# Kernel optimization log

Measured on AMD Instinct MI355X. Metric: run time of the kernel, lower is better.

The kernel has to match this reference:

```python
import jax, jax.numpy as jnp
import numpy as np
from jax import lax

FH, FW = 38, 63          # feature map H,W (600x1000 image, stride 16)
A = 9                    # anchors per location (3 scales x 3 ratios)
POOL = 7                 # cfg.POOLING_SIZE
PRE_NMS, POST_NMS = 6000, 300
NMS_THRESH = 0.7
IM_H, IM_W = 600.0, 1000.0
STRIDE = 16.0


def _make_anchors(h, w, stride=16):
    ratios = np.array([0.5, 1.0, 2.0]); scales = np.array([8.0, 16.0, 32.0])
    base = 16.0; ctr = (base - 1.0) / 2.0
    ws = np.round(np.sqrt(base * base / ratios)); hs = np.round(ws * ratios)
    ws = (ws[:, None] * scales[None, :]).ravel(); hs = (hs[:, None] * scales[None, :]).ravel()
    ba = np.stack([ctr - 0.5 * (ws - 1), ctr - 0.5 * (hs - 1),
                   ctr + 0.5 * (ws - 1), ctr + 0.5 * (hs - 1)], 1)
    sx, sy = np.meshgrid(np.arange(w) * stride, np.arange(h) * stride)
    shifts = np.stack([sx.ravel(), sy.ravel(), sx.ravel(), sy.ravel()], 1)
    return (shifts[:, None, :] + ba[None]).reshape(-1, 4).astype(np.float32)


def _conv(x, w, b, pad):
    y = lax.conv_general_dilated(x, w, (1, 1), pad,
                                 dimension_numbers=('NCHW', 'OIHW', 'NCHW'))
    return y + b[None, :, None, None]


def _bbox_transform_inv(anchors, deltas):
    w = anchors[:, 2] - anchors[:, 0] + 1.0
    h = anchors[:, 3] - anchors[:, 1] + 1.0
    cx = anchors[:, 0] + 0.5 * w
    cy = anchors[:, 1] + 0.5 * h
    dx, dy, dw, dh = deltas[:, 0], deltas[:, 1], deltas[:, 2], deltas[:, 3]
    pcx = dx * w + cx; pcy = dy * h + cy
    pw = jnp.exp(dw) * w; ph = jnp.exp(dh) * h
    return jnp.stack([pcx - 0.5 * pw, pcy - 0.5 * ph,
                      pcx + 0.5 * pw, pcy + 0.5 * ph], 1)


def _nms_keep(boxes, thresh):
    # greedy NMS over score-sorted boxes, fixed-size keep mask
    x1, y1, x2, y2 = boxes[:, 0], boxes[:, 1], boxes[:, 2], boxes[:, 3]
    areas = (x2 - x1 + 1.0) * (y2 - y1 + 1.0)
    iw = jnp.maximum(jnp.minimum(x2[:, None], x2[None, :])
                     - jnp.maximum(x1[:, None], x1[None, :]) + 1.0, 0.0)
    ih = jnp.maximum(jnp.minimum(y2[:, None], y2[None, :])
                     - jnp.maximum(y1[:, None], y1[None, :]) + 1.0, 0.0)
    inter = iw * ih
    iou = inter / (areas[:, None] + areas[None, :] - inter)
    n = boxes.shape[0]; ar = jnp.arange(n)
    def body(i, keep):
        sup = (iou[i] > thresh) & (ar > i) & keep[i]
        return keep & ~sup
    return lax.fori_loop(0, n, body, jnp.ones((n,), bool))


def _crop_and_resize(feat, boxes, crop):
    # feat [C,H,W]; boxes [R,4] normalized (y1,x1,y2,x2); TF crop_and_resize semantics
    C, H, W = feat.shape
    t = jnp.arange(crop, dtype=feat.dtype) / (crop - 1)
    def one(box):
        by1, bx1, by2, bx2 = box
        ys = by1 * (H - 1) + t * (by2 - by1) * (H - 1)
        xs = bx1 * (W - 1) + t * (bx2 - bx1) * (W - 1)
        y0f = jnp.floor(ys); x0f = jnp.floor(xs)
        wy = (ys - y0f)[None, :, None]; wx = (xs - x0f)[None, None, :]
        y0 = jnp.clip(y0f, 0, H - 1).astype(jnp.int32)
        y1i = jnp.clip(y0f + 1, 0, H - 1).astype(jnp.int32)
        x0 = jnp.clip(x0f, 0, W - 1).astype(jnp.int32)
        x1i = jnp.clip(x0f + 1, 0, W - 1).astype(jnp.int32)
        f00 = feat[:, y0][:, :, x0]; f01 = feat[:, y0][:, :, x1i]
        f10 = feat[:, y1i][:, :, x0]; f11 = feat[:, y1i][:, :, x1i]
        return (f00 * (1 - wy) * (1 - wx) + f01 * (1 - wy) * wx
                + f10 * wy * (1 - wx) + f11 * wy * wx)
    return jax.vmap(one)(boxes)


def _forward(net_conv, w_rpn, b_rpn, w_cls, b_cls, w_bbox, b_bbox, anchors):
    # _region_proposal: 3x3 rpn conv + relu, 1x1 cls / bbox heads
    rpn = jax.nn.relu(_conv(net_conv, w_rpn, b_rpn, 'SAME'))
    cls = _conv(rpn, w_cls, b_cls, 'VALID')    # [1,2A,H,W]
    bbox = _conv(rpn, w_bbox, b_bbox, 'VALID')  # [1,4A,H,W]
    # view(1,2,-1,W) softmax: channel a pairs with channel a+A (bg/fg)
    bg, fg = cls[:, :A], cls[:, A:]
    fg_prob = jax.nn.softmax(jnp.stack([bg, fg], axis=1), axis=1)[:, 1]  # [1,A,H,W]
    scores = jnp.transpose(fg_prob, (0, 2, 3, 1)).reshape(-1)            # (H*W*A,)
    deltas = jnp.transpose(bbox, (0, 2, 3, 1)).reshape(-1, 4)
    proposals = _bbox_transform_inv(anchors, deltas)
    proposals = jnp.stack([jnp.clip(proposals[:, 0], 0.0, IM_W - 1.0),
                           jnp.clip(proposals[:, 1], 0.0, IM_H - 1.0),
                           jnp.clip(proposals[:, 2], 0.0, IM_W - 1.0),
                           jnp.clip(proposals[:, 3], 0.0, IM_H - 1.0)], 1)
    # proposal selection is non-differentiable (rois.detach() in original)
    scores_sg = lax.stop_gradient(scores)
    props_sg = lax.stop_gradient(proposals)
    _, order = lax.top_k(scores_sg, PRE_NMS)
    boxes = props_sg[order]
    keep = _nms_keep(boxes, NMS_THRESH)
    idx = jnp.sort(jnp.where(keep, jnp.arange(PRE_NMS), PRE_NMS))[:POST_NMS]
    rois = boxes[jnp.minimum(idx, PRE_NMS - 1)]  # [300,4] (x1,y1,x2,y2)
    # _crop_pool_layer with max_pool=True: crop to 14x14 then 2x2 max pool
    H, W = net_conv.shape[2], net_conv.shape[3]
    x1 = rois[:, 0] / STRIDE; y1 = rois[:, 1] / STRIDE
    x2 = rois[:, 2] / STRIDE; y2 = rois[:, 3] / STRIDE
    norm = jnp.stack([y1 / (H - 1), x1 / (W - 1), y2 / (H - 1), x2 / (W - 1)], 1)
    crops = _crop_and_resize(net_conv[0], norm, 2 * POOL)  # [300,C,14,14]
    R, C = crops.shape[0], crops.shape[1]
    return crops.reshape(R, C, POOL, 2, POOL, 2).max(axis=(3, 5))  # [300,C,7,7]


def setup_inputs():
    key = jax.random.key(0)
    ks = jax.random.split(key, 4)
    net_conv = jax.random.normal(ks[0], (1, 512, FH, FW), jnp.float32)
    w_rpn = jax.random.normal(ks[1], (512, 512, 3, 3), jnp.float32) * 0.01
    b_rpn = jnp.zeros((512,), jnp.float32)
    w_cls = jax.random.normal(ks[2], (2 * A, 512, 1, 1), jnp.float32) * 0.01
    b_cls = jnp.zeros((2 * A,), jnp.float32)
    w_bbox = jax.random.normal(ks[3], (4 * A, 512, 1, 1), jnp.float32) * 0.01
    b_bbox = jnp.zeros((4 * A,), jnp.float32)
    anchors = jnp.asarray(_make_anchors(FH, FW))
    return {"net_conv": net_conv, "w_rpn": w_rpn, "b_rpn": b_rpn,
            "w_cls": w_cls, "b_cls": b_cls, "w_bbox": w_bbox,
            "b_bbox": b_bbox, "anchors": anchors}


def reference(net_conv, w_rpn, b_rpn, w_cls, b_cls, w_bbox, b_bbox, anchors):
    return _forward(net_conv, w_rpn, b_rpn, w_cls, b_cls, w_bbox, b_bbox, anchors)
```

## Files before the change

### kernel.cpp

```cpp
#include <hip/hip_runtime.h>
#include <stdint.h>

#define NPOS 2394
#define CIN 512
#define KK 4608
#define NANCH 21546
#define PRE 6000
#define POST 300
#define NWORD 94
#define NQ 8
#define QLEN 2694
#define FEATT_BYTES 4902912

#define OFF_BH    0
#define OFF_BL    4718592
#define OFF_P0    9437184
#define OFF_SBOX  9437184
#define OFF_KEEP  9533440
#define OFF_DIAG  9633792
#define OFF_P1    14340096
#define OFF_KEYS  19243008
#define OFF_PROP  19415552
#define OFF_RPART 19760384
#define OFF_FPH   20450048
#define OFF_FPL   23179264

typedef _Float16 half8 __attribute__((ext_vector_type(8)));
typedef float f32x4 __attribute__((ext_vector_type(4)));

__device__ __forceinline__ void gload16(const void* g, void* l) {
    __builtin_amdgcn_global_load_lds((const __attribute__((address_space(1))) void*)g,
                                     (__attribute__((address_space(3))) void*)l, 16, 0, 0);
}

__device__ __forceinline__ unsigned long long rl64(unsigned long long v, int l) {
    union { unsigned long long q; unsigned int d[2]; } s; s.q = v;
    unsigned int lo = __builtin_amdgcn_readlane(s.d[0], l);
    unsigned int hi = __builtin_amdgcn_readlane(s.d[1], l);
    return ((unsigned long long)hi << 32) | (unsigned long long)lo;
}

__global__ __launch_bounds__(256) void k_transpose_feat(const float* __restrict__ in,
                                                        float* __restrict__ featT) {
    __shared__ float tl[32][33];
    int tx = threadIdx.x & 31, tg = threadIdx.x >> 5;
    int posBase = blockIdx.x * 32, ciBase = blockIdx.y * 32;
#pragma unroll
    for (int j = 0; j < 4; ++j) {
        int ci = ciBase + tg + j * 8;
        int pos = posBase + tx;
        tl[tg + j * 8][tx] = (pos < NPOS) ? in[(size_t)ci * NPOS + pos] : 0.f;
    }
    __syncthreads();
#pragma unroll
    for (int j = 0; j < 4; ++j) {
        int pos = posBase + tg + j * 8;
        int ci = ciBase + tx;
        if (pos < NPOS) featT[(size_t)pos * 512 + ci] = tl[tx][tg + j * 8];
    }
}

__global__ void k_pad_split(const float* __restrict__ featT,
                            _Float16* __restrict__ FPH, _Float16* __restrict__ FPL) {
    int idx = blockIdx.x * 256 + threadIdx.x;
    int ci = idx & 511;
    int rc = idx >> 9;
    int hp = rc / 65, wp = rc - hp * 65;
    int h = hp - 1, w = wp - 1;
    float a = 0.f;
    if ((unsigned)h < 38u && (unsigned)w < 63u)
        a = featT[(size_t)(h * 63 + w) * 512 + ci] * 16.f;
    _Float16 ah = (_Float16)a;
    _Float16 al = (_Float16)(a - (float)ah);
    FPH[idx] = ah; FPL[idx] = al;
}

__global__ void k_prep_wf16(const float* __restrict__ w,
                            _Float16* __restrict__ BH, _Float16* __restrict__ BL) {
    int idx = blockIdx.x * 256 + threadIdx.x;
    int co = idx / KK;
    int rem = idx - co * KK;
    int p = rem >> 9;
    int ci = rem & 511;
    float b = w[(co * CIN + ci) * 9 + p] * 128.f;
    _Float16 bh = (_Float16)b;
    _Float16 bl = (_Float16)(b - (float)bh);
    BH[idx] = bh; BL[idx] = bl;
}

__global__ __launch_bounds__(256, 3) void k_conv3_mfma(
    const _Float16* __restrict__ FPH, const _Float16* __restrict__ FPL,
    const _Float16* __restrict__ BHp, const _Float16* __restrict__ BLp,
    float* __restrict__ P0, float* __restrict__ P1)
{
    __shared__ __align__(16) char lds[49152];
    const int t = threadIdx.x;
    const int wave = t >> 6, lane = t & 63;
    const int posBase = blockIdx.x * 128;
    const int coBase  = blockIdx.y * 64;
    const int z = blockIdx.z;
    float* __restrict__ P = z ? P1 : P0;
    const int wm = wave >> 1, wn = wave & 1;
    const int lr = lane & 15, lg = lane >> 4;

    int addrA[4][2], addrB[2][2];
#pragma unroll
    for (int m = 0; m < 4; ++m) {
        int row = wm * 64 + m * 16 + lr;
        int x = row & 7;
        addrA[m][0] = row * 128 + ((lg ^ x) << 4);
        addrA[m][1] = row * 128 + (((4 + lg) ^ x) << 4);
    }
#pragma unroll
    for (int n = 0; n < 2; ++n) {
        int row = wn * 32 + n * 16 + lr;
        int x = row & 7;
        addrB[n][0] = 32768 + row * 128 + ((lg ^ x) << 4);
        addrB[n][1] = 32768 + row * 128 + (((4 + lg) ^ x) << 4);
    }

    int baseA[4], ldsAo[4];
#pragma unroll
    for (int s = 0; s < 4; ++s) {
        int row = (wave * 4 + s) * 8 + (lane >> 3);
        int pos = posBase + row;
        int h = pos / 63;
        int w = pos - h * 63;
        int swz = ((lane & 7) ^ (row & 7)) * 8;
        baseA[s] = (h * 65 + w) * 512 + swz;
        ldsAo[s] = (wave * 4 + s) * 1024 + lane * 16;
    }
    int baseB[2], ldsBo[2];
#pragma unroll
    for (int s = 0; s < 2; ++s) {
        int row = (wave * 2 + s) * 8 + (lane >> 3);
        int swz = ((lane & 7) ^ (row & 7)) * 8;
        baseB[s] = (coBase + row) * KK + swz;
        ldsBo[s] = 32768 + (wave * 2 + s) * 1024 + lane * 16;
    }

    f32x4 acc[4][2];
#pragma unroll
    for (int m = 0; m < 4; ++m)
#pragma unroll
        for (int n = 0; n < 2; ++n) acc[m][n] = (f32x4){0.f, 0.f, 0.f, 0.f};

    const int kbeg = z * 2304;
    for (int step = 0; step < 36; ++step) {
        int k0 = kbeg + step * 64;
        int p = k0 >> 9;
        int ci0 = k0 & 511;
        int kh = p / 3;
        int kw = p - kh * 3;
        int dA = (kh * 65 + kw) * 512 + ci0;
#pragma unroll
        for (int s = 0; s < 4; ++s) {
            int so = baseA[s] + dA;
            gload16(FPH + so, lds + ldsAo[s]);
            gload16(FPL + so, lds + 16384 + ldsAo[s]);
        }
#pragma unroll
        for (int s = 0; s < 2; ++s) {
            int so = baseB[s] + k0;
            gload16(BHp + so, lds + ldsBo[s]);
            gload16(BLp + so, lds + 8192 + ldsBo[s]);
        }
        __syncthreads();
#pragma unroll
        for (int ks = 0; ks < 2; ++ks) {
            half8 aH[4], aL[4], bH[2], bL[2];
#pragma unroll
            for (int m = 0; m < 4; ++m) {
                aH[m] = *(const half8*)(lds + addrA[m][ks]);
                aL[m] = *(const half8*)(lds + 16384 + addrA[m][ks]);
            }
#pragma unroll
            for (int n = 0; n < 2; ++n) {
                bH[n] = *(const half8*)(lds + addrB[n][ks]);
                bL[n] = *(const half8*)(lds + 8192 + addrB[n][ks]);
            }
#pragma unroll
            for (int m = 0; m < 4; ++m)
#pragma unroll
                for (int n = 0; n < 2; ++n) {
                    acc[m][n] = __builtin_amdgcn_mfma_f32_16x16x32_f16(aH[m], bH[n], acc[m][n], 0, 0, 0);
                    acc[m][n] = __builtin_amdgcn_mfma_f32_16x16x32_f16(aH[m], bL[n], acc[m][n], 0, 0, 0);
                    acc[m][n] = __builtin_amdgcn_mfma_f32_16x16x32_f16(aL[m], bH[n], acc[m][n], 0, 0, 0);
                }
        }
        __syncthreads();
    }

#pragma unroll
    for (int m = 0; m < 4; ++m) {
        int pbase = posBase + wm * 64 + m * 16 + lg * 4;
        int co = coBase + wn * 32 + lr;
#pragma unroll
        for (int r = 0; r < 4; ++r) {
            int pos = pbase + r;
            if (pos < NPOS) {
                P[(size_t)pos * 512 + co]      = acc[m][0][r] * (1.f / 2048.f);
                P[(size_t)pos * 512 + co + 16] = acc[m][1][r] * (1.f / 2048.f);
            }
        }
    }
}

__global__ __launch_bounds__(256) void k_heads(const float* __restrict__ P0,
                                               const float* __restrict__ P1,
                                               const float* __restrict__ brpn,
                                               const float* __restrict__ wcls,
                                               const float* __restrict__ bcls,
                                               const float* __restrict__ wbbox,
                                               const float* __restrict__ bbbox,
                                               const float* __restrict__ anchors,
                                               float* __restrict__ proposals,
                                               unsigned long long* __restrict__ keys) {
    __shared__ float x[512];
    __shared__ float part[54][4];
    __shared__ float logit[54];
    int pos = blockIdx.x;
    int t = threadIdx.x;
    {
        float v0 = P0[(size_t)pos * 512 + t] + P1[(size_t)pos * 512 + t] + brpn[t];
        float v1 = P0[(size_t)pos * 512 + t + 256] + P1[(size_t)pos * 512 + t + 256] + brpn[t + 256];
        x[t] = v0 > 0.f ? v0 : 0.f;
        x[t + 256] = v1 > 0.f ? v1 : 0.f;
    }
    __syncthreads();
    if (t < 216) {
        int o = t >> 2, q = t & 3;
        const float* wr = (o < 18) ? (wcls + o * 512) : (wbbox + (o - 18) * 512);
        float s = 0.f;
        int base = q * 128;
#pragma unroll 4
        for (int k2 = 0; k2 < 128; ++k2) s += x[base + k2] * wr[base + k2];
        part[o][q] = s;
    }
    __syncthreads();
    if (t < 54) {
        float b = (t < 18) ? bcls[t] : bbbox[t - 18];
        logit[t] = part[t][0] + part[t][1] + part[t][2] + part[t][3] + b;
    }
    __syncthreads();
    if (t < 9) {
        int a = t;
        float bg = logit[a], fg = logit[9 + a];
        float score = 1.f / (1.f + expf(bg - fg));
        float dx = logit[18 + 4 * a], dy = logit[19 + 4 * a];
        float dw = logit[20 + 4 * a], dh = logit[21 + 4 * a];
        int idx = pos * 9 + a;
        float ax1 = anchors[idx * 4 + 0], ay1 = anchors[idx * 4 + 1];
        float ax2 = anchors[idx * 4 + 2], ay2 = anchors[idx * 4 + 3];
        float aw = ax2 - ax1 + 1.f, ah = ay2 - ay1 + 1.f;
        float cx = ax1 + 0.5f * aw, cy = ay1 + 0.5f * ah;
        float pcx = dx * aw + cx, pcy = dy * ah + cy;
        float pw = expf(dw) * aw, ph = expf(dh) * ah;
        float x1 = fminf(fmaxf(pcx - 0.5f * pw, 0.f), 999.f);
        float y1 = fminf(fmaxf(pcy - 0.5f * ph, 0.f), 599.f);
        float x2 = fminf(fmaxf(pcx + 0.5f * pw, 0.f), 999.f);
        float y2 = fminf(fmaxf(pcy + 0.5f * ph, 0.f), 599.f);
        proposals[idx * 4 + 0] = x1; proposals[idx * 4 + 1] = y1;
        proposals[idx * 4 + 2] = x2; proposals[idx * 4 + 3] = y2;
        union { float f; unsigned int i; } sv; sv.f = score;
        keys[idx] = (((unsigned long long)sv.i) << 32) |
                    (unsigned long long)(0xFFFFFFFFu - (unsigned)idx);
    }
}

__global__ __launch_bounds__(256) void k_rank_partial(const unsigned long long* __restrict__ keys,
                                                      unsigned int* __restrict__ rpart) {
    __shared__ unsigned long long kc[1024];
    int i = blockIdx.x * 256 + threadIdx.x;
    int q = blockIdx.y;
    unsigned long long myk = (i < NANCH) ? keys[i] : 0xFFFFFFFFFFFFFFFFull;
    int j0 = q * QLEN;
    int j1 = j0 + QLEN; if (j1 > NANCH) j1 = NANCH;
    unsigned int cnt = 0;
    for (int base = j0; base < j1; base += 1024) {
        int nload = j1 - base; if (nload > 1024) nload = 1024;
        __syncthreads();
        for (int u = threadIdx.x; u < 1024; u += 256)
            kc[u] = (base + u < j1) ? keys[base + u] : 0ull;
        __syncthreads();
        for (int u = 0; u < nload; ++u)
            cnt += (kc[u] > myk) ? 1u : 0u;
    }
    if (i < NANCH) rpart[i * NQ + q] = cnt;
}

__global__ void k_zero_aux(float* __restrict__ sboxes, unsigned long long* __restrict__ diag4) {
    int i = blockIdx.x * 256 + threadIdx.x;
    diag4[i] = 0ull;
    if (i < PRE * 4) sboxes[i] = 0.f;
}

__global__ void k_rank_scatter(const unsigned int* __restrict__ rpart,
                               const float* __restrict__ proposals,
                               float* __restrict__ sboxes) {
    int i = blockIdx.x * 256 + threadIdx.x;
    if (i >= NANCH) return;
    unsigned int r = 0;
#pragma unroll
    for (int q = 0; q < NQ; q++) r += rpart[i * NQ + q];
    if (r < PRE) {
        sboxes[r * 4 + 0] = proposals[i * 4 + 0];
        sboxes[r * 4 + 1] = proposals[i * 4 + 1];
        sboxes[r * 4 + 2] = proposals[i * 4 + 2];
        sboxes[r * 4 + 3] = proposals[i * 4 + 3];
    }
}

__global__ __launch_bounds__(64) void k_nms_mask(const float* __restrict__ sboxes,
                                                 unsigned long long* __restrict__ mask,
                                                 unsigned long long* __restrict__ diag4) {
    __shared__ float bx[64][4];
    int ib = blockIdx.x, jb = blockIdx.y;
    int lane = threadIdx.x;
    int j = jb * 64 + lane;
    if (j < PRE) {
        bx[lane][0] = sboxes[j * 4 + 0]; bx[lane][1] = sboxes[j * 4 + 1];
        bx[lane][2] = sboxes[j * 4 + 2]; bx[lane][3] = sboxes[j * 4 + 3];
    } else {
        bx[lane][0] = 3e8f; bx[lane][1] = 3e8f; bx[lane][2] = 3e8f; bx[lane][3] = 3e8f;
    }
    __syncthreads();
    int i = ib * 64 + lane;
    if (i >= PRE) return;
    float x1 = sboxes[i * 4 + 0], y1 = sboxes[i * 4 + 1];
    float x2 = sboxes[i * 4 + 2], y2 = sboxes[i * 4 + 3];
    float ar = (x2 - x1 + 1.f) * (y2 - y1 + 1.f);
    unsigned long long bits = 0;
#pragma unroll 4
    for (int u = 0; u < 64; u++) {
        int j2 = jb * 64 + u;
        float iw = fminf(x2, bx[u][2]) - fmaxf(x1, bx[u][0]) + 1.f;
        float ih = fminf(y2, bx[u][3]) - fmaxf(y1, bx[u][1]) + 1.f;
        iw = fmaxf(iw, 0.f); ih = fmaxf(ih, 0.f);
        float inter = iw * ih;
        float arj = (bx[u][2] - bx[u][0] + 1.f) * (bx[u][3] - bx[u][1] + 1.f);
        float iou = inter / (ar + arj - inter);
        if (iou > 0.7f && j2 > i) bits |= (1ull << u);
    }
    mask[(size_t)i * NWORD + jb] = bits;
    if ((jb >> 2) == (ib >> 2)) diag4[(size_t)i * 4 + (jb & 3)] = bits;
}

#define NSB 24
#define SBW 256
#define NSLOT 20
__global__ __launch_bounds__(64) void k_nms_scan(const unsigned long long* __restrict__ mask,
                                                 const unsigned long long* __restrict__ diag4,
                                                 int* __restrict__ keep) {
    __shared__ __align__(16) unsigned long long tile[2][SBW * 4];
    __shared__ __align__(16) char ldsrow[NSLOT * 1024];
    __shared__ int ldsk[POST];
    const int lane = threadIdx.x;
    const char* dg = (const char*)diag4;

    for (int c = 0; c < 8; ++c)
        gload16(dg + c * 1024 + (size_t)lane * 16, (char*)tile[0] + c * 1024);

    unsigned long long rem0 = 0, rem1 = 0;
    int nk = 0, npend = 0;

    for (int sb = 0; sb < NSB; ++sb) {
        if (sb + 1 < NSB) {
            const char* src = dg + (size_t)(sb + 1) * 8192;
            char* dst = (char*)tile[(sb + 1) & 1];
            for (int c = 0; c < 8; ++c)
                gload16(src + c * 1024 + (size_t)lane * 16, dst + c * 1024);
            asm volatile("s_waitcnt vmcnt(8)" ::: "memory");
        } else {
            asm volatile("s_waitcnt vmcnt(0)" ::: "memory");
        }
        __builtin_amdgcn_sched_barrier(0);

        for (int q = 0; q < npend; ++q) {
            const unsigned long long* lr = (const unsigned long long*)(ldsrow + q * 1024);
            rem0 |= lr[lane];
            if (lane < NWORD - 64) rem1 |= lr[64 + lane];
        }
        npend = 0;

        const unsigned long long* tl = tile[sb & 1];
        unsigned long long d[4][4];
#pragma unroll
        for (int q = 0; q < 4; ++q) {
            ulonglong2 e0 = *(const ulonglong2*)&tl[(q * 64 + lane) * 4];
            ulonglong2 e1 = *(const ulonglong2*)&tl[(q * 64 + lane) * 4 + 2];
            d[q][0] = e0.x; d[q][1] = e0.y; d[q][2] = e1.x; d[q][3] = e1.y;
        }

        const int w0 = 4 * sb;
        const int base = sb * SBW;
        unsigned long long rmw[4];
#pragma unroll
        for (int j = 0; j < 4; ++j) {
            int w = w0 + j;
            rmw[j] = (w < 64) ? rl64(rem0, w) : ((w < NWORD) ? rl64(rem1, w - 64) : ~0ull);
        }

#pragma unroll
        for (int p = 0; p < 4; ++p) {
            int w = w0 + p;
            if (w >= NWORD) break;
            const unsigned long long valid = (w == NWORD - 1) ? ((1ull << 48) - 1) : ~0ull;
            unsigned long long above = ~0ull;
            unsigned long long keptm = 0;
            for (;;) {
                unsigned long long a = ~rmw[p] & valid & above;
                if (!a) break;
                int u = (int)(__ffsll((long long)a) - 1);
                keptm |= 1ull << u;
                ++nk;
#pragma unroll
                for (int j = p; j < 4; ++j) rmw[j] |= rl64(d[p][j], u);
                if (nk == POST) break;
                above = (u == 63) ? 0ull : (~0ull << (u + 1));
            }
            unsigned long long bits = keptm;
            int nkb = nk - __builtin_popcountll(keptm);
            while (bits) {
                int u = (int)(__ffsll((long long)bits) - 1); bits &= bits - 1;
                int i = base + p * 64 + u;
                if (lane == 0) ldsk[nkb] = i;
                ++nkb;
                if (npend == NSLOT) {
                    asm volatile("s_waitcnt vmcnt(0)" ::: "memory");
                    __builtin_amdgcn_sched_barrier(0);
                    for (int q = 0; q < NSLOT; ++q) {
                        const unsigned long long* lr = (const unsigned long long*)(ldsrow + q * 1024);
                        rem0 |= lr[lane];
                        if (lane < NWORD - 64) rem1 |= lr[64 + lane];
                    }
                    npend = 0;
                }
                gload16((const char*)(mask + (size_t)i * NWORD) + (size_t)lane * 16,
                        ldsrow + npend * 1024);
                ++npend;
            }
            if (nk >= POST) goto done;
        }
    }
done:
    asm volatile("s_waitcnt vmcnt(0)" ::: "memory");
    for (int k2 = lane; k2 < POST; k2 += 64)
        keep[k2] = (k2 < nk) ? ldsk[k2] : PRE - 1;
}

__global__ __launch_bounds__(256) void k_gather_rois(const float* sboxes, const int* keep,
                                                     float* outF) {
    int t = threadIdx.x;
    float4 box[2];
    int nr = 0;
    for (int r = t; r < POST; r += 256) {
        int ki = keep[r];
        if (ki < 0) ki = 0; if (ki > PRE - 1) ki = PRE - 1;
        box[nr++] = *reinterpret_cast<const float4*>(sboxes + ki * 4);
    }
    __syncthreads();
    nr = 0;
    for (int r = t; r < POST; r += 256) {
        float4 b = box[nr++];
#pragma unroll
        for (int cg = 0; cg < 8; ++cg)
            *reinterpret_cast<float4*>(outF + (size_t)(r * 512 + cg * 64) * 49) = b;
    }
}

__global__ __launch_bounds__(256) void k_crop_fast(const float* __restrict__ featT,
                                                   float* out) {
    __shared__ float lds[4][49 * 65];
    int r = blockIdx.x;
    int w = threadIdx.x >> 6, lane = threadIdx.x & 63;
    int cg = blockIdx.y * 4 + w;
    int c = cg * 64 + lane;
    float* chunk = out + (size_t)(r * 512 + cg * 64) * 49;
    const float4 b = *reinterpret_cast<const float4*>(chunk);
    float x1 = b.x, y1 = b.y, x2 = b.z, y2 = b.w;
    float by1 = (y1 / 16.f) / 37.f, bx1 = (x1 / 16.f) / 62.f;
    float by2 = (y2 / 16.f) / 37.f, bx2 = (x2 / 16.f) / 62.f;
    float dyn = by2 - by1, dxn = bx2 - bx1;
    for (int e = 0; e < 49; ++e) {
        int oy = e / 7, ox = e - oy * 7;
        float vv[4];
#pragma unroll
        for (int dy = 0; dy < 2; ++dy) {
            int sy = 2 * oy + dy;
            float ty = (float)sy / 13.f;
            float ys = by1 * 37.f + (ty * dyn) * 37.f;
            float yf = floorf(ys);
            float wy = ys - yf;
            int y0  = (int)fminf(fmaxf(yf, 0.f), 37.f);
            int y1i = (int)fminf(fmaxf(yf + 1.f, 0.f), 37.f);
#pragma unroll
            for (int dxx = 0; dxx < 2; ++dxx) {
                int sx = 2 * ox + dxx;
                float tx = (float)sx / 13.f;
                float xs = bx1 * 62.f + (tx * dxn) * 62.f;
                float xf = floorf(xs);
                float wx = xs - xf;
                int x0  = (int)fminf(fmaxf(xf, 0.f), 62.f);
                int x1i = (int)fminf(fmaxf(xf + 1.f, 0.f), 62.f);
                float f00 = featT[(size_t)(y0 * 63 + x0) * 512 + c];
                float f01 = featT[(size_t)(y0 * 63 + x1i) * 512 + c];
                float f10 = featT[(size_t)(y1i * 63 + x0) * 512 + c];
                float f11 = featT[(size_t)(y1i * 63 + x1i) * 512 + c];
                vv[dy * 2 + dxx] = f00 * (1.f - wy) * (1.f - wx) + f01 * (1.f - wy) * wx +
                                   f10 * wy * (1.f - wx) + f11 * wy * wx;
            }
        }
        lds[w][e * 65 + lane] = fmaxf(fmaxf(vv[0], vv[1]), fmaxf(vv[2], vv[3]));
    }
    __syncthreads();
    for (int i = lane; i < 64 * 49; i += 64) {
        int cl = i / 49, e = i - cl * 49;
        chunk[i] = lds[w][e * 65 + cl];
    }
}

__global__ __launch_bounds__(64) void k_crop_slow(const float* __restrict__ net,
                                                  float* out) {
    int r = blockIdx.x, cg = blockIdx.y;
    int lane = threadIdx.x;
    int c = cg * 64 + lane;
    const float4 b = *reinterpret_cast<const float4*>(out + (size_t)(r * 512 + cg * 64) * 49);
    float x1 = b.x, y1 = b.y, x2 = b.z, y2 = b.w;
    float by1 = (y1 / 16.f) / 37.f, bx1 = (x1 / 16.f) / 62.f;
    float by2 = (y2 / 16.f) / 37.f, bx2 = (x2 / 16.f) / 62.f;
    float dyn = by2 - by1, dxn = bx2 - bx1;
    const float* fc = net + (size_t)c * NPOS;
    float* orow = out + ((size_t)r * 512 + c) * 49;
    for (int e = 0; e < 49; ++e) {
        int oy = e / 7, ox = e - oy * 7;
        float vv[4];
#pragma unroll
        for (int dy = 0; dy < 2; ++dy) {
            int sy = 2 * oy + dy;
            float ty = (float)sy / 13.f;
            float ys = by1 * 37.f + (ty * dyn) * 37.f;
            float yf = floorf(ys);
            float wy = ys - yf;
            int y0  = (int)fminf(fmaxf(yf, 0.f), 37.f);
            int y1i = (int)fminf(fmaxf(yf + 1.f, 0.f), 37.f);
#pragma unroll
            for (int dxx = 0; dxx < 2; ++dxx) {
                int sx = 2 * ox + dxx;
                float tx = (float)sx / 13.f;
                float xs = bx1 * 62.f + (tx * dxn) * 62.f;
                float xf = floorf(xs);
                float wx = xs - xf;
                int x0  = (int)fminf(fmaxf(xf, 0.f), 62.f);
                int x1i = (int)fminf(fmaxf(xf + 1.f, 0.f), 62.f);
                float f00 = fc[y0 * 63 + x0];
                float f01 = fc[y0 * 63 + x1i];
                float f10 = fc[y1i * 63 + x0];
                float f11 = fc[y1i * 63 + x1i];
                vv[dy * 2 + dxx] = f00 * (1.f - wy) * (1.f - wx) + f01 * (1.f - wy) * wx +
                                   f10 * wy * (1.f - wx) + f11 * wy * wx;
            }
        }
        orow[e] = fmaxf(fmaxf(vv[0], vv[1]), fmaxf(vv[2], vv[3]));
    }
}

extern "C" void kernel_launch(void* const* d_in, const int* in_sizes, int n_in,
                              void* d_out, int out_size, void* d_ws, size_t ws_size,
                              hipStream_t stream) {
    auto find = [&](int count, int fallback) {
        for (int i = 0; i < n_in; ++i) if (in_sizes[i] == count) return i;
        return fallback;
    };
    const float* net   = (const float*)d_in[find(NPOS * CIN, 0)];
    const float* wrpn  = (const float*)d_in[find(512 * KK, 1)];
    const float* brpn  = (const float*)d_in[find(512, 2)];
    const float* wcls  = (const float*)d_in[find(18 * 512, 3)];
    const float* bcls  = (const float*)d_in[find(18, 4)];
    const float* wbbox = (const float*)d_in[find(36 * 512, 5)];
    const float* bbbox = (const float*)d_in[find(36, 6)];
    const float* anch  = (const float*)d_in[find(NANCH * 4, 7)];

    char* ob = (char*)d_out;
    _Float16* BH             = (_Float16*)(ob + OFF_BH);
    _Float16* BL             = (_Float16*)(ob + OFF_BL);
    unsigned long long* mask = (unsigned long long*)(ob + OFF_BH);
    float* P0                = (float*)(ob + OFF_P0);
    float* P1                = (float*)(ob + OFF_P1);
    float* sboxes            = (float*)(ob + OFF_SBOX);
    int* keep                = (int*)(ob + OFF_KEEP);
    unsigned long long* diag4= (unsigned long long*)(ob + OFF_DIAG);
    unsigned long long* keys = (unsigned long long*)(ob + OFF_KEYS);
    float* proposals         = (float*)(ob + OFF_PROP);
    unsigned int* rpart      = (unsigned int*)(ob + OFF_RPART);
    _Float16* FPH            = (_Float16*)(ob + OFF_FPH);
    _Float16* FPL            = (_Float16*)(ob + OFF_FPL);
    float* outF              = (float*)d_out;

    const bool ws_ok = (ws_size >= (size_t)FEATT_BYTES);
    float* featT = ws_ok ? (float*)d_ws : (float*)(ob + OFF_P0);

    hipLaunchKernelGGL(k_transpose_feat, dim3(75, 16), dim3(256), 0, stream, net, featT);
    hipLaunchKernelGGL(k_pad_split, dim3(5330), dim3(256), 0, stream, featT, FPH, FPL);
    hipLaunchKernelGGL(k_prep_wf16, dim3(9216), dim3(256), 0, stream, wrpn, BH, BL);
    hipLaunchKernelGGL(k_conv3_mfma, dim3(19, 8, 2), dim3(256), 0, stream, FPH, FPL, BH, BL, P0, P1);
    hipLaunchKernelGGL(k_heads, dim3(NPOS), dim3(256), 0, stream, P0, P1, brpn, wcls, bcls, wbbox, bbbox, anch, proposals, keys);
    hipLaunchKernelGGL(k_rank_partial, dim3(85, NQ), dim3(256), 0, stream, keys, rpart);
    hipLaunchKernelGGL(k_zero_aux, dim3(96), dim3(256), 0, stream, sboxes, diag4);
    hipLaunchKernelGGL(k_rank_scatter, dim3(85), dim3(256), 0, stream, rpart, proposals, sboxes);
    hipLaunchKernelGGL(k_nms_mask, dim3(NWORD, NWORD), dim3(64), 0, stream, sboxes, mask, diag4);
    hipLaunchKernelGGL(k_nms_scan, dim3(1), dim3(64), 0, stream, mask, diag4, keep);
    hipLaunchKernelGGL(k_gather_rois, dim3(1), dim3(256), 0, stream, sboxes, keep, outF);
    if (ws_ok)
        hipLaunchKernelGGL(k_crop_fast, dim3(POST, 2), dim3(256), 0, stream, featT, outF);
    else
        hipLaunchKernelGGL(k_crop_slow, dim3(POST, 8), dim3(64), 0, stream, net, outF);
}
```

Measured before the change: 410.5 us.

## Split conv K dimension three ways with XCD-aware block swizzle

The 3x3 conv GEMM goes from a 2-way to a 3-way split-K, giving 456 blocks instead of 304 and better filling the device's compute units. A 1-D grid with an (bid&7)*57 remap spreads neighbouring tiles across the XCDs. The heads kernel now sums three partial buffers, which adds global memory traffic. The workspace offsets are rearranged so the extra partial buffer fits, with NMS scratch moved to regions that are no longer in use by then.

```diff
diff --git a/kernel.cpp b/kernel.cpp
--- a/kernel.cpp
+++ b/kernel.cpp
@@ -14,16 +14,18 @@
 
 #define OFF_BH    0
 #define OFF_BL    4718592
-#define OFF_P0    9437184
-#define OFF_SBOX  9437184
-#define OFF_KEEP  9533440
-#define OFF_DIAG  9633792
-#define OFF_P1    14340096
-#define OFF_KEYS  19243008
-#define OFF_PROP  19415552
-#define OFF_RPART 19760384
-#define OFF_FPH   20450048
-#define OFF_FPL   23179264
+#define OFF_FPH   9437184
+#define OFF_FPL   12166144
+#define OFF_P0    14895104
+#define OFF_P1    19798016
+#define OFF_P2    24700928
+#define OFF_KEYS  0
+#define OFF_PROP  180224
+#define OFF_RPART 532480
+#define OFF_SBOX  1228800
+#define OFF_KEEP  1327104
+#define OFF_DIAG  1335296
+#define OFF_MASK  4718592
 
 typedef _Float16 half8 __attribute__((ext_vector_type(8)));
 typedef float f32x4 __attribute__((ext_vector_type(4)));
@@ -91,15 +93,22 @@
 __global__ __launch_bounds__(256, 3) void k_conv3_mfma(
     const _Float16* __restrict__ FPH, const _Float16* __restrict__ FPL,
     const _Float16* __restrict__ BHp, const _Float16* __restrict__ BLp,
-    float* __restrict__ P0, float* __restrict__ P1)
+    float* __restrict__ P0, float* __restrict__ P1, float* __restrict__ P2)
 {
     __shared__ __align__(16) char lds[49152];
     const int t = threadIdx.x;
     const int wave = t >> 6, lane = t & 63;
-    const int posBase = blockIdx.x * 128;
-    const int coBase  = blockIdx.y * 64;
-    const int z = blockIdx.z;
-    float* __restrict__ P = z ? P1 : P0;
+
+    const int bid = blockIdx.x;
+    const int swz = (bid & 7) * 57 + (bid >> 3);
+    const int z = swz / 152;
+    const int rem = swz - z * 152;
+    const int coB = rem / 19;
+    const int posB = rem - coB * 19;
+    const int posBase = posB * 128;
+    const int coBase  = coB * 64;
+    float* __restrict__ P = (z == 0) ? P0 : ((z == 1) ? P1 : P2);
+
     const int wm = wave >> 1, wn = wave & 1;
     const int lr = lane & 15, lg = lane >> 4;
 
@@ -126,16 +135,16 @@
         int pos = posBase + row;
         int h = pos / 63;
         int w = pos - h * 63;
-        int swz = ((lane & 7) ^ (row & 7)) * 8;
-        baseA[s] = (h * 65 + w) * 512 + swz;
+        int swzb = ((lane & 7) ^ (row & 7)) * 8;
+        baseA[s] = (h * 65 + w) * 512 + swzb;
         ldsAo[s] = (wave * 4 + s) * 1024 + lane * 16;
     }
     int baseB[2], ldsBo[2];
 #pragma unroll
     for (int s = 0; s < 2; ++s) {
         int row = (wave * 2 + s) * 8 + (lane >> 3);
-        int swz = ((lane & 7) ^ (row & 7)) * 8;
-        baseB[s] = (coBase + row) * KK + swz;
+        int swzb = ((lane & 7) ^ (row & 7)) * 8;
+        baseB[s] = (coBase + row) * KK + swzb;
         ldsBo[s] = 32768 + (wave * 2 + s) * 1024 + lane * 16;
     }
 
@@ -145,8 +154,8 @@
 #pragma unroll
         for (int n = 0; n < 2; ++n) acc[m][n] = (f32x4){0.f, 0.f, 0.f, 0.f};
 
-    const int kbeg = z * 2304;
-    for (int step = 0; step < 36; ++step) {
+    const int kbeg = z * 1536;
+    for (int step = 0; step < 24; ++step) {
         int k0 = kbeg + step * 64;
         int p = k0 >> 9;
         int ci0 = k0 & 511;
@@ -208,6 +217,7 @@
 
 __global__ __launch_bounds__(256) void k_heads(const float* __restrict__ P0,
                                                const float* __restrict__ P1,
+                                               const float* __restrict__ P2,
                                                const float* __restrict__ brpn,
                                                const float* __restrict__ wcls,
                                                const float* __restrict__ bcls,
@@ -222,8 +232,9 @@
     int pos = blockIdx.x;
     int t = threadIdx.x;
     {
-        float v0 = P0[(size_t)pos * 512 + t] + P1[(size_t)pos * 512 + t] + brpn[t];
-        float v1 = P0[(size_t)pos * 512 + t + 256] + P1[(size_t)pos * 512 + t + 256] + brpn[t + 256];
+        size_t o = (size_t)pos * 512 + t;
+        float v0 = P0[o] + P1[o] + P2[o] + brpn[t];
+        float v1 = P0[o + 256] + P1[o + 256] + P2[o + 256] + brpn[t + 256];
         x[t] = v0 > 0.f ? v0 : 0.f;
         x[t + 256] = v1 > 0.f ? v1 : 0.f;
     }
@@ -584,17 +595,18 @@
     char* ob = (char*)d_out;
     _Float16* BH             = (_Float16*)(ob + OFF_BH);
     _Float16* BL             = (_Float16*)(ob + OFF_BL);
-    unsigned long long* mask = (unsigned long long*)(ob + OFF_BH);
+    _Float16* FPH            = (_Float16*)(ob + OFF_FPH);
+    _Float16* FPL            = (_Float16*)(ob + OFF_FPL);
     float* P0                = (float*)(ob + OFF_P0);
     float* P1                = (float*)(ob + OFF_P1);
+    float* P2                = (float*)(ob + OFF_P2);
+    unsigned long long* keys = (unsigned long long*)(ob + OFF_KEYS);
+    float* proposals         = (float*)(ob + OFF_PROP);
+    unsigned int* rpart      = (unsigned int*)(ob + OFF_RPART);
     float* sboxes            = (float*)(ob + OFF_SBOX);
     int* keep                = (int*)(ob + OFF_KEEP);
     unsigned long long* diag4= (unsigned long long*)(ob + OFF_DIAG);
-    unsigned long long* keys = (unsigned long long*)(ob + OFF_KEYS);
-    float* proposals         = (float*)(ob + OFF_PROP);
-    unsigned int* rpart      = (unsigned int*)(ob + OFF_RPART);
-    _Float16* FPH            = (_Float16*)(ob + OFF_FPH);
-    _Float16* FPL            = (_Float16*)(ob + OFF_FPL);
+    unsigned long long* mask = (unsigned long long*)(ob + OFF_MASK);
     float* outF              = (float*)d_out;
 
     const bool ws_ok = (ws_size >= (size_t)FEATT_BYTES);
@@ -603,8 +615,8 @@
     hipLaunchKernelGGL(k_transpose_feat, dim3(75, 16), dim3(256), 0, stream, net, featT);
     hipLaunchKernelGGL(k_pad_split, dim3(5330), dim3(256), 0, stream, featT, FPH, FPL);
     hipLaunchKernelGGL(k_prep_wf16, dim3(9216), dim3(256), 0, stream, wrpn, BH, BL);
-    hipLaunchKernelGGL(k_conv3_mfma, dim3(19, 8, 2), dim3(256), 0, stream, FPH, FPL, BH, BL, P0, P1);
-    hipLaunchKernelGGL(k_heads, dim3(NPOS), dim3(256), 0, stream, P0, P1, brpn, wcls, bcls, wbbox, bbbox, anch, proposals, keys);
+    hipLaunchKernelGGL(k_conv3_mfma, dim3(456), dim3(256), 0, stream, FPH, FPL, BH, BL, P0, P1, P2);
+    hipLaunchKernelGGL(k_heads, dim3(NPOS), dim3(256), 0, stream, P0, P1, P2, brpn, wcls, bcls, wbbox, bbbox, anch, proposals, keys);
     hipLaunchKernelGGL(k_rank_partial, dim3(85, NQ), dim3(256), 0, stream, keys, rpart);
     hipLaunchKernelGGL(k_zero_aux, dim3(96), dim3(256), 0, stream, sboxes, diag4);
     hipLaunchKernelGGL(k_rank_scatter, dim3(85), dim3(256), 0, stream, rpart, proposals, sboxes);
```

New measurement: 386.1 us. 5.9% less time.
